# Optimization experiments

Hardware: AMD Instinct MI355X
Metric: run time of the kernel (lower is better)

Reference implementation:

```python
import jax, jax.numpy as jnp
import numpy as np

S, D, E = 16384, 4096, 64
CAPACITY_FACTOR = 1.25  # training mode
CAPACITY = int(CAPACITY_FACTOR * S / E)  # 320


def setup_inputs() -> dict:
    key = jax.random.key(0)
    kx, kw = jax.random.split(key)
    x = jax.random.normal(kx, (S, D), dtype=jnp.float32)
    W_g = jax.random.normal(kw, (E, D), dtype=jnp.float32) * (1.0 / np.sqrt(D))
    return {"x": x, "W_g": W_g}


def reference(x, W_g):
    # Router GEMM + softmax.  x: [S, D], W_g: [E, D] (nn.Linear weight layout).
    S_ = x.shape[0]
    E_ = W_g.shape[0]
    logits = x @ W_g.T                       # [S, E]
    gates = jax.nn.softmax(logits, axis=-1)  # [S, E]

    # Top-2 experts per token (topk is constant across the original per-token loop,
    # so we compute it once).
    vals, idx = jax.lax.top_k(gates, 2)
    g1, g2 = vals[:, 0], vals[:, 1]          # [S]
    e1, e2 = idx[:, 0], idx[:, 1]            # [S] int32
    denom = g1 + g2
    g1n = g1 / denom                         # normalized top-1 gate
    g2n = g2 / denom                         # normalized top-2 gate

    # Pass 1: top-1 dispatch, capacity-limited, serialized in token order.
    # cumsum of one-hot gives each token its 1-indexed position within its expert.
    m1 = jax.nn.one_hot(e1, E_, dtype=gates.dtype)              # [S, E]
    pos1 = jnp.sum(jnp.cumsum(m1, axis=0) * m1, axis=-1)        # [S]
    keep1 = pos1 <= CAPACITY                                    # [S] bool
    counts1 = jnp.sum(m1 * keep1[:, None].astype(gates.dtype), axis=0)  # [E]

    # Pass 2: top-2 dispatch with random keep prob (rnd < 2*g2n), capacity-limited
    # against the counts remaining after pass 1, again serialized in token order.
    rnd = jax.random.uniform(jax.random.key(1), (S_,), dtype=gates.dtype)
    want2 = rnd < 2.0 * g2n                                     # [S] bool
    m2 = jax.nn.one_hot(e2, E_, dtype=gates.dtype) * want2[:, None].astype(gates.dtype)
    pos2 = jnp.sum(jnp.cumsum(m2, axis=0) * m2, axis=-1)        # [S]
    keep2 = want2 & (pos2 <= (CAPACITY - counts1)[e2])          # [S] bool

    rows = jnp.arange(S_)
    combine = jnp.zeros_like(gates)
    combine = combine.at[rows, e1].set(jnp.where(keep1, g1n, 0.0))
    combine = combine.at[rows, e2].set(jnp.where(keep2, g2n, 0.0))
    return combine
```

## Files before the change

### kernel.cpp

```cpp
#include <hip/hip_runtime.h>
#include <stdint.h>

#define S 16384
#define D 4096
#define NE 64
#define CAP 320
#define WPB 4
#define KSPLIT 8
#define KCH (D / KSPLIT)
#define KSTEPS (KCH / 16)
#define NKS (D / 16)
#define K2ROWS 128
#define NB (S / K2ROWS)

typedef _Float16 f16x8 __attribute__((ext_vector_type(8)));
typedef float f32x16 __attribute__((ext_vector_type(16)));

__device__ __forceinline__ uint32_t rotl32(uint32_t v, int n) {
  return (v << n) | (v >> (32 - n));
}

__device__ uint32_t threefry_bits(int i) {
  const uint32_t k0 = 0u, k1 = 1u;
  const uint32_t ks2 = k0 ^ k1 ^ 0x1BD11BDAu;
  uint32_t x0 = 0u + k0;
  uint32_t x1 = (uint32_t)i + k1;
#define TFR(R) { x0 += x1; x1 = rotl32(x1, R); x1 ^= x0; }
  TFR(13) TFR(15) TFR(26) TFR(6)
  x0 += k1;  x1 += ks2 + 1u;
  TFR(17) TFR(29) TFR(16) TFR(24)
  x0 += ks2; x1 += k0 + 2u;
  TFR(13) TFR(15) TFR(26) TFR(6)
  x0 += k0;  x1 += k1 + 3u;
  TFR(17) TFR(29) TFR(16) TFR(24)
  x0 += k1;  x1 += ks2 + 4u;
  TFR(13) TFR(15) TFR(26) TFR(6)
  x0 += ks2; x1 += k0 + 5u;
#undef TFR
  return x0 ^ x1;
}

__global__ __launch_bounds__(256) void k0_packw(const float* __restrict__ Wg,
                                                f16x8* __restrict__ WH,
                                                f16x8* __restrict__ WL) {
  const int tid = blockIdx.x * 256 + threadIdx.x;
  const int lane = tid & 63;
  const int t = (tid >> 6) & 1;
  const int ks = tid >> 7;
  const int col = 32 * t + (lane & 31);
  const int k0 = ks * 16 + 8 * (lane >> 5);
  const float* wp = Wg + (size_t)col * D + k0;
  f16x8 h, l;
#pragma unroll
  for (int j = 0; j < 8; ++j) {
    const float w = wp[j];
    const _Float16 wh = (_Float16)w;
    const float r = (w - (float)wh) * 4096.0f;
    h[j] = wh;
    l[j] = (_Float16)r;
  }
  WH[tid] = h;
  WL[tid] = l;
}

#define CVT1(J, F)                                                     \
  { const float f_ = (F); const _Float16 h_ = (_Float16)f_;            \
    ah[J] = h_; al[J] = (_Float16)((f_ - (float)h_) * 4096.0f); }

#define KSTEP(X0, X1, BH0, BH1, BL0, BL1)                                    \
  {                                                                          \
    f16x8 ah, al;                                                            \
    CVT1(0, (X0).x) CVT1(1, (X0).y) CVT1(2, (X0).z) CVT1(3, (X0).w)          \
    CVT1(4, (X1).x) CVT1(5, (X1).y) CVT1(6, (X1).z) CVT1(7, (X1).w)          \
    acc00 = __builtin_amdgcn_mfma_f32_32x32x16_f16(ah, BH0, acc00, 0, 0, 0); \
    acc10 = __builtin_amdgcn_mfma_f32_32x32x16_f16(al, BH0, acc10, 0, 0, 0); \
    acc10 = __builtin_amdgcn_mfma_f32_32x32x16_f16(ah, BL0, acc10, 0, 0, 0); \
    acc01 = __builtin_amdgcn_mfma_f32_32x32x16_f16(ah, BH1, acc01, 0, 0, 0); \
    acc11 = __builtin_amdgcn_mfma_f32_32x32x16_f16(al, BH1, acc11, 0, 0, 0); \
    acc11 = __builtin_amdgcn_mfma_f32_32x32x16_f16(ah, BL1, acc11, 0, 0, 0); \
  }

__global__ __launch_bounds__(256) void k1_logits(const float* __restrict__ x,
                                                 const f16x8* __restrict__ WH,
                                                 const f16x8* __restrict__ WL,
                                                 float* __restrict__ part) {
  __shared__ float lsum[WPB][32][64];
  const int w = threadIdx.x >> 6;
  const int lane = threadIdx.x & 63;
  const int rg = blockIdx.x >> 1;
  const int kh = blockIdx.x & 1;
  const int rowBase = rg * 32;
  const int row = rowBase + (lane & 31);
  const int kidx = kh * 4 + w;
  const float* xp = x + (size_t)row * D + kidx * KCH + (lane >> 5) * 8;
  const float4* xq = (const float4*)xp;
  const int ks0 = kidx * KSTEPS;

  f32x16 acc00, acc01, acc10, acc11;
#pragma unroll
  for (int r = 0; r < 16; ++r) { acc00[r] = 0.0f; acc01[r] = 0.0f; acc10[r] = 0.0f; acc11[r] = 0.0f; }

  float4 xa0 = xq[0], xa1 = xq[1];
  size_t fiA = (size_t)ks0 * 128 + lane;
  f16x8 bha0 = WH[fiA], bha1 = WH[fiA + 64];
  f16x8 bla0 = WL[fiA], bla1 = WL[fiA + 64];

  for (int s = 0; s < KSTEPS; s += 2) {
    const size_t fiB = (size_t)(ks0 + s + 1) * 128 + lane;
    const float4 xb0 = xq[(s + 1) * 4];
    const float4 xb1 = xq[(s + 1) * 4 + 1];
    const f16x8 bhb0 = WH[fiB], bhb1 = WH[fiB + 64];
    const f16x8 blb0 = WL[fiB], blb1 = WL[fiB + 64];

    KSTEP(xa0, xa1, bha0, bha1, bla0, bla1);

    const int s2 = (s + 2 < KSTEPS) ? (s + 2) : 0;
    const size_t fiA2 = (size_t)(ks0 + s2) * 128 + lane;
    xa0 = xq[s2 * 4]; xa1 = xq[s2 * 4 + 1];
    bha0 = WH[fiA2]; bha1 = WH[fiA2 + 64];
    bla0 = WL[fiA2]; bla1 = WL[fiA2 + 64];

    KSTEP(xb0, xb1, bhb0, bhb1, blb0, blb1);
  }

#pragma unroll
  for (int r = 0; r < 16; ++r) {
    const int lrow = (r & 3) + 8 * (r >> 2) + 4 * (lane >> 5);
    lsum[w][lrow][lane & 31]        = acc00[r] + acc10[r] * (1.0f / 4096.0f);
    lsum[w][lrow][32 + (lane & 31)] = acc01[r] + acc11[r] * (1.0f / 4096.0f);
  }
  __syncthreads();

  {
    const float* p0 = &lsum[0][0][0];
#pragma unroll
    for (int j = 0; j < 8; ++j) {
      const int idx = threadIdx.x + 256 * j;
      const float v = ((p0[idx] + p0[idx + 2048]) + p0[idx + 4096]) + p0[idx + 6144];
      part[((size_t)kh * S + rowBase) * NE + idx] = v;
    }
  }
}

__global__ __launch_bounds__(256) void k1b_reduce(const float* __restrict__ part,
                                                  int* __restrict__ E1, int* __restrict__ E2,
                                                  int* __restrict__ WANT,
                                                  float* __restrict__ G1, float* __restrict__ G2) {
  const int row = blockIdx.x * 4 + (threadIdx.x >> 6);
  const int lane = threadIdx.x & 63;
  float l = 0.0f;
#pragma unroll
  for (int c = 0; c < 2; ++c)
    l += part[((size_t)c * S + row) * NE + lane];

  float m = l;
#pragma unroll
  for (int off = 32; off; off >>= 1) m = fmaxf(m, __shfl_xor(m, off));
  const float ex = expf(l - m);
  float ssum = ex;
#pragma unroll
  for (int off = 32; off; off >>= 1) ssum += __shfl_xor(ssum, off);
  ssum = __shfl(ssum, 0);
  const float gate = ex / ssum;

  float v = gate; int id = lane;
#pragma unroll
  for (int off = 32; off; off >>= 1) {
    float vo = __shfl_xor(v, off); int io = __shfl_xor(id, off);
    if (vo > v || (vo == v && io < id)) { v = vo; id = io; }
  }
  const float g1 = v; const int e1 = id;
  const float gate2 = (lane == e1) ? -1.0f : gate;
  v = gate2; id = lane;
#pragma unroll
  for (int off = 32; off; off >>= 1) {
    float vo = __shfl_xor(v, off); int io = __shfl_xor(id, off);
    if (vo > v || (vo == v && io < id)) { v = vo; id = io; }
  }
  const float g2 = v; const int e2 = id;

  if (lane == 0) {
    const float denom = g1 + g2;
    const float g1n = g1 / denom;
    const float g2n = g2 / denom;
    const uint32_t bits = threefry_bits(row);
    const float rnd = __uint_as_float((bits >> 9) | 0x3f800000u) - 1.0f;
    E1[row] = e1; E2[row] = e2;
    WANT[row] = (rnd < 2.0f * g2n) ? 1 : 0;
    G1[row] = g1n; G2[row] = g2n;
  }
}

__global__ __launch_bounds__(K2ROWS) void k2_rank(const int* __restrict__ E1,
                                                  const int* __restrict__ E2,
                                                  const int* __restrict__ WANT,
                                                  int* __restrict__ LR1, int* __restrict__ LR2,
                                                  int* __restrict__ H1, int* __restrict__ H2) {
  __shared__ unsigned char s1[K2ROWS], s2[K2ROWS];
  __shared__ int h1[NE], h2[NE];
  const int b = blockIdx.x, t = threadIdx.x;
  const int r = b * K2ROWS + t;
  if (t < NE) { h1[t] = 0; h2[t] = 0; }
  const int e1 = E1[r];
  const int e2 = WANT[r] ? E2[r] : NE;
  s1[t] = (unsigned char)e1;
  s2[t] = (unsigned char)e2;
  __syncthreads();
  int r1 = 0, r2 = 0;
  for (int j = 0; j < t; ++j) {
    r1 += (s1[j] == e1);
    r2 += (s2[j] == e2);
  }
  LR1[r] = r1; LR2[r] = r2;
  atomicAdd(&h1[e1], 1);
  if (e2 < NE) atomicAdd(&h2[e2], 1);
  __syncthreads();
  if (t < NE) { H1[b * NE + t] = h1[t]; H2[b * NE + t] = h2[t]; }
}

__global__ __launch_bounds__(256) void k3_prefix(const int* __restrict__ H1,
                                                 const int* __restrict__ H2,
                                                 int* __restrict__ OFF1, int* __restrict__ OFF2,
                                                 int* __restrict__ REM2) {
  __shared__ int sh1[NB * NE], sh2[NB * NE];
  const int t = threadIdx.x;
#pragma unroll
  for (int j = 0; j < 8; ++j) {
    const int i4 = t + 256 * j;
    ((int4*)sh1)[i4] = ((const int4*)H1)[i4];
    ((int4*)sh2)[i4] = ((const int4*)H2)[i4];
  }
  __syncthreads();
  if (t < NE) {
    int run1 = 0, run2 = 0;
    for (int b = 0; b < NB; ++b) {
      OFF1[b * NE + t] = run1; run1 += sh1[b * NE + t];
      OFF2[b * NE + t] = run2; run2 += sh2[b * NE + t];
    }
    REM2[t] = CAP - min(run1, CAP);
  }
}

__global__ __launch_bounds__(256) void k4_write(const int* __restrict__ E1,
                                                const int* __restrict__ E2,
                                                const int* __restrict__ WANT,
                                                const float* __restrict__ G1,
                                                const float* __restrict__ G2,
                                                const int* __restrict__ LR1,
                                                const int* __restrict__ LR2,
                                                const int* __restrict__ OFF1,
                                                const int* __restrict__ OFF2,
                                                const int* __restrict__ REM2,
                                                float* __restrict__ out) {
  const int w = threadIdx.x >> 6, lane = threadIdx.x & 63;
  const int rowBase = blockIdx.x * 16 + w * 4;
#pragma unroll
  for (int i = 0; i < 4; ++i) {
    const int r = rowBase + i;
    const int b = r / K2ROWS;
    const int e1 = E1[r];
    const int pos1 = OFF1[b * NE + e1] + LR1[r] + 1;
    float val = 0.0f;
    if (lane == e1 && pos1 <= CAP) val = G1[r];
    if (WANT[r]) {
      const int e2 = E2[r];
      const int pos2 = OFF2[b * NE + e2] + LR2[r] + 1;
      if (lane == e2 && pos2 <= REM2[e2]) val = G2[r];
    }
    out[(size_t)r * NE + lane] = val;
  }
}

extern "C" void kernel_launch(void* const* d_in, const int* in_sizes, int n_in,
                              void* d_out, int out_size, void* d_ws, size_t ws_size,
                              hipStream_t stream) {
  const float* x  = (const float*)d_in[0];
  const float* Wg = (const float*)d_in[1];
  float* out = (float*)d_out;
  char* ws = (char*)d_ws;

  size_t off = 0;
  float* part = (float*)ws;         off += (size_t)2 * S * NE * 4;
  int*   E1   = (int*)(ws + off);   off += (size_t)S * 4;
  int*   E2   = (int*)(ws + off);   off += (size_t)S * 4;
  int*   WANT = (int*)(ws + off);   off += (size_t)S * 4;
  float* G1   = (float*)(ws + off); off += (size_t)S * 4;
  float* G2   = (float*)(ws + off); off += (size_t)S * 4;
  int*   LR1  = (int*)(ws + off);   off += (size_t)S * 4;
  int*   LR2  = (int*)(ws + off);   off += (size_t)S * 4;
  int*   H1   = (int*)(ws + off);   off += (size_t)NB * NE * 4;
  int*   H2   = (int*)(ws + off);   off += (size_t)NB * NE * 4;
  int*   OFF1 = (int*)(ws + off);   off += (size_t)NB * NE * 4;
  int*   OFF2 = (int*)(ws + off);   off += (size_t)NB * NE * 4;
  int*   REM2 = (int*)(ws + off);   off += (size_t)NE * 4;
  f16x8* WH   = (f16x8*)(ws + off); off += (size_t)NKS * 2 * 64 * sizeof(f16x8);
  f16x8* WL   = (f16x8*)(ws + off); off += (size_t)NKS * 2 * 64 * sizeof(f16x8);

  k0_packw<<<128, 256, 0, stream>>>(Wg, WH, WL);
  k1_logits<<<(S / 32) * 2, 256, 0, stream>>>(x, WH, WL, part);
  k1b_reduce<<<S / 4, 256, 0, stream>>>(part, E1, E2, WANT, G1, G2);
  k2_rank<<<NB, K2ROWS, 0, stream>>>(E1, E2, WANT, LR1, LR2, H1, H2);
  k3_prefix<<<1, 256, 0, stream>>>(H1, H2, OFF1, OFF2, REM2);
  k4_write<<<S / 16, 256, 0, stream>>>(E1, E2, WANT, G1, G2, LR1, LR2, OFF1, OFF2, REM2, out);
}
```

Baseline: 394.4 us.

## Fuse router GEMM with softmax/top-2 and stage x through swizzled LDS

Drops the two-way K split, so one block of four waves covers the full K range for 32 rows. That removes the partial-logit buffer and the separate reduce kernel, and the softmax, top-2 and random-keep step now run in the same kernel. Activation tiles are loaded with coalesced float4 global reads into a double-buffered, XOR-swizzled LDS buffer, replacing the strided per-lane direct loads. The catch is that the grid halves to 512 blocks and LDS use rises to 64KB per block, which may lower occupancy and latency hiding on the memory-bound x read.

```diff
diff --git a/kernel.cpp b/kernel.cpp
--- a/kernel.cpp
+++ b/kernel.cpp
@@ -5,10 +5,10 @@
 #define D 4096
 #define NE 64
 #define CAP 320
-#define WPB 4
-#define KSPLIT 8
-#define KCH (D / KSPLIT)
-#define KSTEPS (KCH / 16)
+#define WQ 4
+#define KCH (D / WQ)
+#define CH 64
+#define NCH (KCH / CH)
 #define NKS (D / 16)
 #define K2ROWS 128
 #define NB (S / K2ROWS)
@@ -80,114 +80,141 @@
     acc11 = __builtin_amdgcn_mfma_f32_32x32x16_f16(ah, BL1, acc11, 0, 0, 0); \
   }
 
-__global__ __launch_bounds__(256) void k1_logits(const float* __restrict__ x,
-                                                 const f16x8* __restrict__ WH,
-                                                 const f16x8* __restrict__ WL,
-                                                 float* __restrict__ part) {
-  __shared__ float lsum[WPB][32][64];
+__global__ __launch_bounds__(256) void k1_fused(const float* __restrict__ x,
+                                                const f16x8* __restrict__ WH,
+                                                const f16x8* __restrict__ WL,
+                                                int* __restrict__ E1, int* __restrict__ E2,
+                                                int* __restrict__ WANT,
+                                                float* __restrict__ G1, float* __restrict__ G2) {
+  __shared__ __align__(16) float xbuf[WQ][2][32][64];
   const int w = threadIdx.x >> 6;
   const int lane = threadIdx.x & 63;
-  const int rg = blockIdx.x >> 1;
-  const int kh = blockIdx.x & 1;
-  const int rowBase = rg * 32;
-  const int row = rowBase + (lane & 31);
-  const int kidx = kh * 4 + w;
-  const float* xp = x + (size_t)row * D + kidx * KCH + (lane >> 5) * 8;
-  const float4* xq = (const float4*)xp;
-  const int ks0 = kidx * KSTEPS;
+  const int rowBase = blockIdx.x * 32;
+  const int srow = lane >> 4;
+  const int scol = (lane & 15) * 4;
+  const int arow = lane & 31;
+  const int ahalf = lane >> 5;
+  const int swzr = (arow & 7) << 2;
+
+  const float* xsrc = x + (size_t)(rowBase + srow) * D + w * KCH + scol;
+  float* mybuf0 = &xbuf[w][0][0][0];
+  float* mybuf1 = &xbuf[w][1][0][0];
+
+  const int sw0 = (0 * 4 + srow) * 64 + (scol ^ (((0 * 4 + srow) & 7) << 2));
+  const int sw1 = (1 * 4 + srow) * 64 + (scol ^ (((1 * 4 + srow) & 7) << 2));
+  const int sw2 = (2 * 4 + srow) * 64 + (scol ^ (((2 * 4 + srow) & 7) << 2));
+  const int sw3 = (3 * 4 + srow) * 64 + (scol ^ (((3 * 4 + srow) & 7) << 2));
+  const int sw4 = (4 * 4 + srow) * 64 + (scol ^ (((4 * 4 + srow) & 7) << 2));
+  const int sw5 = (5 * 4 + srow) * 64 + (scol ^ (((5 * 4 + srow) & 7) << 2));
+  const int sw6 = (6 * 4 + srow) * 64 + (scol ^ (((6 * 4 + srow) & 7) << 2));
+  const int sw7 = (7 * 4 + srow) * 64 + (scol ^ (((7 * 4 + srow) & 7) << 2));
+
+  float4 g0, g1, g2, g3, g4, g5, g6, g7;
+
+#define LDG(C)                                                \
+  g0 = *(const float4*)(xsrc + 0 * 16384 + (C) * CH);         \
+  g1 = *(const float4*)(xsrc + 1 * 16384 + (C) * CH);         \
+  g2 = *(const float4*)(xsrc + 2 * 16384 + (C) * CH);         \
+  g3 = *(const float4*)(xsrc + 3 * 16384 + (C) * CH);         \
+  g4 = *(const float4*)(xsrc + 4 * 16384 + (C) * CH);         \
+  g5 = *(const float4*)(xsrc + 5 * 16384 + (C) * CH);         \
+  g6 = *(const float4*)(xsrc + 6 * 16384 + (C) * CH);         \
+  g7 = *(const float4*)(xsrc + 7 * 16384 + (C) * CH);
+
+#define STW(BUF)                                              \
+  *(float4*)&(BUF)[sw0] = g0; *(float4*)&(BUF)[sw1] = g1;     \
+  *(float4*)&(BUF)[sw2] = g2; *(float4*)&(BUF)[sw3] = g3;     \
+  *(float4*)&(BUF)[sw4] = g4; *(float4*)&(BUF)[sw5] = g5;     \
+  *(float4*)&(BUF)[sw6] = g6; *(float4*)&(BUF)[sw7] = g7;
+
+#define COMPUTE(BUF, C)                                                       \
+  _Pragma("unroll")                                                           \
+  for (int s_ = 0; s_ < 4; ++s_) {                                            \
+    const int kf_ = 16 * s_ + 8 * ahalf;                                      \
+    const float4 xa0 = *(const float4*)&(BUF)[arow * 64 + (kf_ ^ swzr)];      \
+    const float4 xa1 = *(const float4*)&(BUF)[arow * 64 + ((kf_ + 4) ^ swzr)];\
+    const size_t fi = (size_t)(w * 64 + (C) * 4 + s_) * 128 + lane;           \
+    const f16x8 bh0 = WH[fi], bh1 = WH[fi + 64];                              \
+    const f16x8 bl0 = WL[fi], bl1 = WL[fi + 64];                              \
+    KSTEP(xa0, xa1, bh0, bh1, bl0, bl1)                                       \
+  }
 
   f32x16 acc00, acc01, acc10, acc11;
 #pragma unroll
   for (int r = 0; r < 16; ++r) { acc00[r] = 0.0f; acc01[r] = 0.0f; acc10[r] = 0.0f; acc11[r] = 0.0f; }
 
-  float4 xa0 = xq[0], xa1 = xq[1];
-  size_t fiA = (size_t)ks0 * 128 + lane;
-  f16x8 bha0 = WH[fiA], bha1 = WH[fiA + 64];
-  f16x8 bla0 = WL[fiA], bla1 = WL[fiA + 64];
-
-  for (int s = 0; s < KSTEPS; s += 2) {
-    const size_t fiB = (size_t)(ks0 + s + 1) * 128 + lane;
-    const float4 xb0 = xq[(s + 1) * 4];
-    const float4 xb1 = xq[(s + 1) * 4 + 1];
-    const f16x8 bhb0 = WH[fiB], bhb1 = WH[fiB + 64];
-    const f16x8 blb0 = WL[fiB], blb1 = WL[fiB + 64];
-
-    KSTEP(xa0, xa1, bha0, bha1, bla0, bla1);
-
-    const int s2 = (s + 2 < KSTEPS) ? (s + 2) : 0;
-    const size_t fiA2 = (size_t)(ks0 + s2) * 128 + lane;
-    xa0 = xq[s2 * 4]; xa1 = xq[s2 * 4 + 1];
-    bha0 = WH[fiA2]; bha1 = WH[fiA2 + 64];
-    bla0 = WL[fiA2]; bla1 = WL[fiA2 + 64];
-
-    KSTEP(xb0, xb1, bhb0, bhb1, blb0, blb1);
-  }
-
+  LDG(0)
+  STW(mybuf0)
+  for (int cc = 0; cc < NCH; cc += 2) {
+    LDG(cc + 1)
+    COMPUTE(mybuf0, cc)
+    STW(mybuf1)
+    if (cc + 2 < NCH) { LDG(cc + 2) }
+    COMPUTE(mybuf1, cc + 1)
+    if (cc + 2 < NCH) { STW(mybuf0) }
+  }
+
+  float* lsw = &xbuf[0][0][0][0] + w * 4096;
 #pragma unroll
   for (int r = 0; r < 16; ++r) {
-    const int lrow = (r & 3) + 8 * (r >> 2) + 4 * (lane >> 5);
-    lsum[w][lrow][lane & 31]        = acc00[r] + acc10[r] * (1.0f / 4096.0f);
-    lsum[w][lrow][32 + (lane & 31)] = acc01[r] + acc11[r] * (1.0f / 4096.0f);
+    const int lrow = (r & 3) + 8 * (r >> 2) + 4 * ahalf;
+    lsw[lrow * 64 + arow]      = acc00[r] + acc10[r] * (1.0f / 4096.0f);
+    lsw[lrow * 64 + 32 + arow] = acc01[r] + acc11[r] * (1.0f / 4096.0f);
   }
   __syncthreads();
 
   {
-    const float* p0 = &lsum[0][0][0];
+    float* base = &xbuf[0][0][0][0];
 #pragma unroll
     for (int j = 0; j < 8; ++j) {
       const int idx = threadIdx.x + 256 * j;
-      const float v = ((p0[idx] + p0[idx + 2048]) + p0[idx + 4096]) + p0[idx + 6144];
-      part[((size_t)kh * S + rowBase) * NE + idx] = v;
-    }
-  }
-}
-
-__global__ __launch_bounds__(256) void k1b_reduce(const float* __restrict__ part,
-                                                  int* __restrict__ E1, int* __restrict__ E2,
-                                                  int* __restrict__ WANT,
-                                                  float* __restrict__ G1, float* __restrict__ G2) {
-  const int row = blockIdx.x * 4 + (threadIdx.x >> 6);
-  const int lane = threadIdx.x & 63;
-  float l = 0.0f;
-#pragma unroll
-  for (int c = 0; c < 2; ++c)
-    l += part[((size_t)c * S + row) * NE + lane];
-
-  float m = l;
-#pragma unroll
-  for (int off = 32; off; off >>= 1) m = fmaxf(m, __shfl_xor(m, off));
-  const float ex = expf(l - m);
-  float ssum = ex;
-#pragma unroll
-  for (int off = 32; off; off >>= 1) ssum += __shfl_xor(ssum, off);
-  ssum = __shfl(ssum, 0);
-  const float gate = ex / ssum;
-
-  float v = gate; int id = lane;
-#pragma unroll
-  for (int off = 32; off; off >>= 1) {
-    float vo = __shfl_xor(v, off); int io = __shfl_xor(id, off);
-    if (vo > v || (vo == v && io < id)) { v = vo; id = io; }
-  }
-  const float g1 = v; const int e1 = id;
-  const float gate2 = (lane == e1) ? -1.0f : gate;
-  v = gate2; id = lane;
-#pragma unroll
-  for (int off = 32; off; off >>= 1) {
-    float vo = __shfl_xor(v, off); int io = __shfl_xor(id, off);
-    if (vo > v || (vo == v && io < id)) { v = vo; id = io; }
-  }
-  const float g2 = v; const int e2 = id;
-
-  if (lane == 0) {
-    const float denom = g1 + g2;
-    const float g1n = g1 / denom;
-    const float g2n = g2 / denom;
-    const uint32_t bits = threefry_bits(row);
-    const float rnd = __uint_as_float((bits >> 9) | 0x3f800000u) - 1.0f;
-    E1[row] = e1; E2[row] = e2;
-    WANT[row] = (rnd < 2.0f * g2n) ? 1 : 0;
-    G1[row] = g1n; G2[row] = g2n;
+      base[idx] = ((base[idx] + base[idx + 4096]) + base[idx + 8192]) + base[idx + 12288];
+    }
+  }
+  __syncthreads();
+
+  const float* lsum0 = &xbuf[0][0][0][0];
+  for (int rr = 0; rr < 8; ++rr) {
+    const int lrow = w * 8 + rr;
+    const int grow = rowBase + lrow;
+    const float l = lsum0[lrow * 64 + lane];
+
+    float m = l;
+#pragma unroll
+    for (int off = 32; off; off >>= 1) m = fmaxf(m, __shfl_xor(m, off));
+    const float ex = expf(l - m);
+    float ssum = ex;
+#pragma unroll
+    for (int off = 32; off; off >>= 1) ssum += __shfl_xor(ssum, off);
+    ssum = __shfl(ssum, 0);
+    const float gate = ex / ssum;
+
+    float v = gate; int id = lane;
+#pragma unroll
+    for (int off = 32; off; off >>= 1) {
+      float vo = __shfl_xor(v, off); int io = __shfl_xor(id, off);
+      if (vo > v || (vo == v && io < id)) { v = vo; id = io; }
+    }
+    const float g1v = v; const int e1 = id;
+    const float gate2 = (lane == e1) ? -1.0f : gate;
+    v = gate2; id = lane;
+#pragma unroll
+    for (int off = 32; off; off >>= 1) {
+      float vo = __shfl_xor(v, off); int io = __shfl_xor(id, off);
+      if (vo > v || (vo == v && io < id)) { v = vo; id = io; }
+    }
+    const float g2v = v; const int e2 = id;
+
+    if (lane == 0) {
+      const float denom = g1v + g2v;
+      const float g1n = g1v / denom;
+      const float g2n = g2v / denom;
+      const uint32_t bits = threefry_bits(grow);
+      const float rnd = __uint_as_float((bits >> 9) | 0x3f800000u) - 1.0f;
+      E1[grow] = e1; E2[grow] = e2;
+      WANT[grow] = (rnd < 2.0f * g2n) ? 1 : 0;
+      G1[grow] = g1n; G2[grow] = g2n;
+    }
   }
 }
 
@@ -280,7 +307,6 @@
   char* ws = (char*)d_ws;
 
   size_t off = 0;
-  float* part = (float*)ws;         off += (size_t)2 * S * NE * 4;
   int*   E1   = (int*)(ws + off);   off += (size_t)S * 4;
   int*   E2   = (int*)(ws + off);   off += (size_t)S * 4;
   int*   WANT = (int*)(ws + off);   off += (size_t)S * 4;
@@ -297,8 +323,7 @@
   f16x8* WL   = (f16x8*)(ws + off); off += (size_t)NKS * 2 * 64 * sizeof(f16x8);
 
   k0_packw<<<128, 256, 0, stream>>>(Wg, WH, WL);
-  k1_logits<<<(S / 32) * 2, 256, 0, stream>>>(x, WH, WL, part);
-  k1b_reduce<<<S / 4, 256, 0, stream>>>(part, E1, E2, WANT, G1, G2);
+  k1_fused<<<S / 32, 256, 0, stream>>>(x, WH, WL, E1, E2, WANT, G1, G2);
   k2_rank<<<NB, K2ROWS, 0, stream>>>(E1, E2, WANT, LR1, LR2, H1, H2);
   k3_prefix<<<1, 256, 0, stream>>>(H1, H2, OFF1, OFF2, REM2);
   k4_write<<<S / 16, 256, 0, stream>>>(E1, E2, WANT, G1, G2, LR1, LR2, OFF1, OFF2, REM2, out);
```

Measured after the change: 416.6 us. 5.6% more time.

## Split K four ways and batch x loads in unrolled groups of eight

Applied to the files above, without the earlier changes.

The router GEMM grid now splits K into four block-level chunks instead of two, so each wave handles 256 K elements instead of 512. Inside a wave the loop is fully unrolled: sixteen float4 loads of x are issued up front, converted to hi/lo fp16 pairs, and then eight MFMA steps run behind a sched_barrier. The aim is more memory-level parallelism and more blocks in flight to hide HBM latency on the x stream. In exchange, the partial-logit buffer and the reduce kernel's reads double, and register pressure rises from holding sixteen f16x8 fragments.

```diff
diff --git a/kernel.cpp b/kernel.cpp
--- a/kernel.cpp
+++ b/kernel.cpp
@@ -5,10 +5,8 @@
 #define D 4096
 #define NE 64
 #define CAP 320
-#define WPB 4
-#define KSPLIT 8
-#define KCH (D / KSPLIT)
-#define KSTEPS (KCH / 16)
+#define KSPLIT 4
+#define KCH 256
 #define NKS (D / 16)
 #define K2ROWS 128
 #define NB (S / K2ROWS)
@@ -63,71 +61,81 @@
   WL[tid] = l;
 }
 
-#define CVT1(J, F)                                                     \
+#define CVT1(AH, AL, J, F)                                             \
   { const float f_ = (F); const _Float16 h_ = (_Float16)f_;            \
-    ah[J] = h_; al[J] = (_Float16)((f_ - (float)h_) * 4096.0f); }
-
-#define KSTEP(X0, X1, BH0, BH1, BL0, BL1)                                    \
-  {                                                                          \
-    f16x8 ah, al;                                                            \
-    CVT1(0, (X0).x) CVT1(1, (X0).y) CVT1(2, (X0).z) CVT1(3, (X0).w)          \
-    CVT1(4, (X1).x) CVT1(5, (X1).y) CVT1(6, (X1).z) CVT1(7, (X1).w)          \
-    acc00 = __builtin_amdgcn_mfma_f32_32x32x16_f16(ah, BH0, acc00, 0, 0, 0); \
-    acc10 = __builtin_amdgcn_mfma_f32_32x32x16_f16(al, BH0, acc10, 0, 0, 0); \
-    acc10 = __builtin_amdgcn_mfma_f32_32x32x16_f16(ah, BL0, acc10, 0, 0, 0); \
-    acc01 = __builtin_amdgcn_mfma_f32_32x32x16_f16(ah, BH1, acc01, 0, 0, 0); \
-    acc11 = __builtin_amdgcn_mfma_f32_32x32x16_f16(al, BH1, acc11, 0, 0, 0); \
-    acc11 = __builtin_amdgcn_mfma_f32_32x32x16_f16(ah, BL1, acc11, 0, 0, 0); \
+    (AH)[J] = h_; (AL)[J] = (_Float16)((f_ - (float)h_) * 4096.0f); }
+
+#define CVT8(SD, XA, XB)                                               \
+  CVT1(ah##SD, al##SD, 0, (XA).x) CVT1(ah##SD, al##SD, 1, (XA).y)      \
+  CVT1(ah##SD, al##SD, 2, (XA).z) CVT1(ah##SD, al##SD, 3, (XA).w)      \
+  CVT1(ah##SD, al##SD, 4, (XB).x) CVT1(ah##SD, al##SD, 5, (XB).y)      \
+  CVT1(ah##SD, al##SD, 6, (XB).z) CVT1(ah##SD, al##SD, 7, (XB).w)
+
+#define BSTEP(SD, KSG)                                                        \
+  {                                                                           \
+    const size_t fi = (size_t)(KSG) * 128 + lane;                             \
+    const f16x8 bh0 = WH[fi], bh1 = WH[fi + 64];                              \
+    const f16x8 bl0 = WL[fi], bl1 = WL[fi + 64];                              \
+    acc00 = __builtin_amdgcn_mfma_f32_32x32x16_f16(ah##SD, bh0, acc00, 0, 0, 0); \
+    acc10 = __builtin_amdgcn_mfma_f32_32x32x16_f16(al##SD, bh0, acc10, 0, 0, 0); \
+    acc10 = __builtin_amdgcn_mfma_f32_32x32x16_f16(ah##SD, bl0, acc10, 0, 0, 0); \
+    acc01 = __builtin_amdgcn_mfma_f32_32x32x16_f16(ah##SD, bh1, acc01, 0, 0, 0); \
+    acc11 = __builtin_amdgcn_mfma_f32_32x32x16_f16(al##SD, bh1, acc11, 0, 0, 0); \
+    acc11 = __builtin_amdgcn_mfma_f32_32x32x16_f16(ah##SD, bl1, acc11, 0, 0, 0); \
   }
 
 __global__ __launch_bounds__(256) void k1_logits(const float* __restrict__ x,
                                                  const f16x8* __restrict__ WH,
                                                  const f16x8* __restrict__ WL,
                                                  float* __restrict__ part) {
-  __shared__ float lsum[WPB][32][64];
+  __shared__ float lsum[4][32][64];
   const int w = threadIdx.x >> 6;
   const int lane = threadIdx.x & 63;
-  const int rg = blockIdx.x >> 1;
-  const int kh = blockIdx.x & 1;
+  const int rg = blockIdx.x >> 2;
+  const int kq = blockIdx.x & 3;
   const int rowBase = rg * 32;
-  const int row = rowBase + (lane & 31);
-  const int kidx = kh * 4 + w;
-  const float* xp = x + (size_t)row * D + kidx * KCH + (lane >> 5) * 8;
-  const float4* xq = (const float4*)xp;
-  const int ks0 = kidx * KSTEPS;
+  const int arow = lane & 31;
+  const int ahalf = lane >> 5;
+  const int sixt = kq * 4 + w;
+  const float4* xq = (const float4*)(x + (size_t)(rowBase + arow) * D + sixt * KCH + ahalf * 8);
+  const int ks0 = sixt * 16;
 
   f32x16 acc00, acc01, acc10, acc11;
 #pragma unroll
   for (int r = 0; r < 16; ++r) { acc00[r] = 0.0f; acc01[r] = 0.0f; acc10[r] = 0.0f; acc11[r] = 0.0f; }
 
-  float4 xa0 = xq[0], xa1 = xq[1];
-  size_t fiA = (size_t)ks0 * 128 + lane;
-  f16x8 bha0 = WH[fiA], bha1 = WH[fiA + 64];
-  f16x8 bla0 = WL[fiA], bla1 = WL[fiA + 64];
-
-  for (int s = 0; s < KSTEPS; s += 2) {
-    const size_t fiB = (size_t)(ks0 + s + 1) * 128 + lane;
-    const float4 xb0 = xq[(s + 1) * 4];
-    const float4 xb1 = xq[(s + 1) * 4 + 1];
-    const f16x8 bhb0 = WH[fiB], bhb1 = WH[fiB + 64];
-    const f16x8 blb0 = WL[fiB], blb1 = WL[fiB + 64];
-
-    KSTEP(xa0, xa1, bha0, bha1, bla0, bla1);
-
-    const int s2 = (s + 2 < KSTEPS) ? (s + 2) : 0;
-    const size_t fiA2 = (size_t)(ks0 + s2) * 128 + lane;
-    xa0 = xq[s2 * 4]; xa1 = xq[s2 * 4 + 1];
-    bha0 = WH[fiA2]; bha1 = WH[fiA2 + 64];
-    bla0 = WL[fiA2]; bla1 = WL[fiA2 + 64];
-
-    KSTEP(xb0, xb1, bhb0, bhb1, blb0, blb1);
-  }
+  f16x8 ah0, ah1, ah2, ah3, ah4, ah5, ah6, ah7;
+  f16x8 al0, al1, al2, al3, al4, al5, al6, al7;
+
+  {
+    const float4 x0 = xq[0],  x1 = xq[1],  x2 = xq[4],  x3 = xq[5];
+    const float4 x4 = xq[8],  x5 = xq[9],  x6 = xq[12], x7 = xq[13];
+    const float4 x8 = xq[16], x9 = xq[17], x10 = xq[20], x11 = xq[21];
+    const float4 x12 = xq[24], x13 = xq[25], x14 = xq[28], x15 = xq[29];
+    CVT8(0, x0, x1)   CVT8(1, x2, x3)   CVT8(2, x4, x5)   CVT8(3, x6, x7)
+    CVT8(4, x8, x9)   CVT8(5, x10, x11) CVT8(6, x12, x13) CVT8(7, x14, x15)
+  }
+  __builtin_amdgcn_sched_barrier(0);
+  BSTEP(0, ks0 + 0) BSTEP(1, ks0 + 1) BSTEP(2, ks0 + 2) BSTEP(3, ks0 + 3)
+  BSTEP(4, ks0 + 4) BSTEP(5, ks0 + 5) BSTEP(6, ks0 + 6) BSTEP(7, ks0 + 7)
+
+  {
+    const float4 x0 = xq[32], x1 = xq[33], x2 = xq[36], x3 = xq[37];
+    const float4 x4 = xq[40], x5 = xq[41], x6 = xq[44], x7 = xq[45];
+    const float4 x8 = xq[48], x9 = xq[49], x10 = xq[52], x11 = xq[53];
+    const float4 x12 = xq[56], x13 = xq[57], x14 = xq[60], x15 = xq[61];
+    CVT8(0, x0, x1)   CVT8(1, x2, x3)   CVT8(2, x4, x5)   CVT8(3, x6, x7)
+    CVT8(4, x8, x9)   CVT8(5, x10, x11) CVT8(6, x12, x13) CVT8(7, x14, x15)
+  }
+  __builtin_amdgcn_sched_barrier(0);
+  BSTEP(0, ks0 + 8)  BSTEP(1, ks0 + 9)  BSTEP(2, ks0 + 10) BSTEP(3, ks0 + 11)
+  BSTEP(4, ks0 + 12) BSTEP(5, ks0 + 13) BSTEP(6, ks0 + 14) BSTEP(7, ks0 + 15)
 
 #pragma unroll
   for (int r = 0; r < 16; ++r) {
-    const int lrow = (r & 3) + 8 * (r >> 2) + 4 * (lane >> 5);
-    lsum[w][lrow][lane & 31]        = acc00[r] + acc10[r] * (1.0f / 4096.0f);
-    lsum[w][lrow][32 + (lane & 31)] = acc01[r] + acc11[r] * (1.0f / 4096.0f);
+    const int lrow = (r & 3) + 8 * (r >> 2) + 4 * ahalf;
+    lsum[w][lrow][arow]      = acc00[r] + acc10[r] * (1.0f / 4096.0f);
+    lsum[w][lrow][32 + arow] = acc01[r] + acc11[r] * (1.0f / 4096.0f);
   }
   __syncthreads();
 
@@ -137,7 +145,7 @@
     for (int j = 0; j < 8; ++j) {
       const int idx = threadIdx.x + 256 * j;
       const float v = ((p0[idx] + p0[idx + 2048]) + p0[idx + 4096]) + p0[idx + 6144];
-      part[((size_t)kh * S + rowBase) * NE + idx] = v;
+      part[((size_t)kq * S + rowBase) * NE + idx] = v;
     }
   }
 }
@@ -150,7 +158,7 @@
   const int lane = threadIdx.x & 63;
   float l = 0.0f;
 #pragma unroll
-  for (int c = 0; c < 2; ++c)
+  for (int c = 0; c < KSPLIT; ++c)
     l += part[((size_t)c * S + row) * NE + lane];
 
   float m = l;
@@ -280,7 +288,7 @@
   char* ws = (char*)d_ws;
 
   size_t off = 0;
-  float* part = (float*)ws;         off += (size_t)2 * S * NE * 4;
+  float* part = (float*)ws;         off += (size_t)KSPLIT * S * NE * 4;
   int*   E1   = (int*)(ws + off);   off += (size_t)S * 4;
   int*   E2   = (int*)(ws + off);   off += (size_t)S * 4;
   int*   WANT = (int*)(ws + off);   off += (size_t)S * 4;
@@ -297,7 +305,7 @@
   f16x8* WL   = (f16x8*)(ws + off); off += (size_t)NKS * 2 * 64 * sizeof(f16x8);
 
   k0_packw<<<128, 256, 0, stream>>>(Wg, WH, WL);
-  k1_logits<<<(S / 32) * 2, 256, 0, stream>>>(x, WH, WL, part);
+  k1_logits<<<(S / 32) * KSPLIT, 256, 0, stream>>>(x, WH, WL, part);
   k1b_reduce<<<S / 4, 256, 0, stream>>>(part, E1, E2, WANT, G1, G2);
   k2_rank<<<NB, K2ROWS, 0, stream>>>(E1, E2, WANT, LR1, LR2, H1, H2);
   k3_prefix<<<1, 256, 0, stream>>>(H1, H2, OFF1, OFF2, REM2);
```

Measured after the change: 402.9 us. 1.02x slower.
